# Kernel optimization log

Hardware: AMD Instinct MI355X
Metric: run time of the kernel (lower is better)

Reference implementation:

```python
import jax, jax.numpy as jnp
import numpy as np

K = 16          # neighbors per query (args.k)
EPS_NORM = 1e-5  # LayerNorm / BatchNorm eps (torch default)


def _knn_edges(xyz, B, n):
    # batch-aware kNN: equal-sized batches, edges never cross batch boundary
    x = xyz.reshape(B, n, 3)
    d2 = jnp.sum((x[:, :, None, :] - x[:, None, :, :]) ** 2, -1)   # [B,n,n]
    _, idx = jax.lax.top_k(-d2, K)                                 # [B,n,K] local neighbor ids
    col = (idx + (jnp.arange(B) * n)[:, None, None]).reshape(-1)   # source (neighbor) [E]
    row = jnp.repeat(jnp.arange(B * n), K)                         # target (query)    [E]
    return row, col


def _forward(support_xyz, batch_index, features, lang_features, mask_flattened,
             W1, b1, ln_g, ln_b, W2, b2,
             Wl1, bl1, bn_g, bn_b, Wl2, bl2,
             Wr1, br1, Wr2, br2, row, col):
    N = support_xyz.shape[0]
    B, L, Fl = lang_features.shape
    # feat_encoder: Linear -> LayerNorm -> ReLU -> Linear
    h = features @ W1 + b1
    mu = h.mean(-1, keepdims=True)
    var = ((h - mu) ** 2).mean(-1, keepdims=True)
    h = (h - mu) / jnp.sqrt(var + EPS_NORM) * ln_g + ln_b
    feats = jax.nn.relu(h) @ W2 + b2                               # [N,F]
    # lang_encoder: Linear -> BatchNorm1d (batch statistics) -> ReLU -> Linear
    hl = lang_features.reshape(B * L, Fl) @ Wl1 + bl1
    mul = hl.mean(0)
    varl = ((hl - mul) ** 2).mean(0)
    hl = (hl - mul) / jnp.sqrt(varl + EPS_NORM) * bn_g + bn_b
    lang = (jax.nn.relu(hl) @ Wl2 + bl2).reshape(B, L, -1)         # [B,L,F]
    lang_flat = lang[batch_index]                                  # [N,L,F]
    # per-point / per-token attention logits
    atten = jnp.einsum('nf,nlf->nl', feats, lang_flat)             # [N,L]
    # segment softmax over incoming kNN edges (CenterOp max / add)
    attenmax = jax.ops.segment_max(atten[col], row, num_segments=N, indices_are_sorted=True)
    a = jnp.exp(atten[col] - attenmax[row])                        # [E,L]
    attensum = jax.ops.segment_sum(a, row, num_segments=N, indices_are_sorted=True)
    # CenterConv message
    att = a / attensum[row] * mask_flattened[row]                  # [E,L]
    att = att / (att.sum(-1, keepdims=True) + 1e-7)
    ctx = jnp.einsum('el,elf->ef', att, lang_flat[col])            # [E,F] attended lang feat
    xi, xj = support_xyz[row], support_xyz[col]
    d = xi - xj
    nrm = jnp.sqrt(jnp.sum(d * d, -1, keepdims=True) + 1e-12)
    ew = jnp.concatenate([xi, xj, d, nrm], -1)                     # [E,10]
    ew = jax.nn.relu(ew @ Wr1 + br1) @ Wr2 + br2                   # [E,F] rel_encoder
    msg = feats[col] * ctx * ew                                    # [E,F]
    rel = jax.ops.segment_sum(msg, row, num_segments=N, indices_are_sorted=True)
    return feats + rel


def setup_inputs() -> dict:
    key = jax.random.key(0)
    ks = jax.random.split(key, 12)
    B, n, L = 4, 1024, 16
    N = B * n
    Fv, Fl, F = 256, 768, 128
    def w(k, shp, fan):
        return jax.random.normal(k, shp, jnp.float32) / np.sqrt(fan).astype(np.float32)
    mask = (jax.random.uniform(ks[3], (N, L)) < 0.8).astype(jnp.float32).at[:, 0].set(1.0)
    return {
        'support_xyz': jax.random.normal(ks[0], (N, 3), jnp.float32),
        'batch_index': jnp.repeat(jnp.arange(B), n),
        'features': jax.random.normal(ks[1], (N, Fv), jnp.float32),
        'lang_features': jax.random.normal(ks[2], (B, L, Fl), jnp.float32),
        'mask_flattened': mask,
        'W1': w(ks[4], (Fv, F), Fv), 'b1': jnp.zeros(F, jnp.float32),
        'ln_g': jnp.ones(F, jnp.float32), 'ln_b': jnp.zeros(F, jnp.float32),
        'W2': w(ks[5], (F, F), F), 'b2': jnp.zeros(F, jnp.float32),
        'Wl1': w(ks[6], (Fl, F), Fl), 'bl1': jnp.zeros(F, jnp.float32),
        'bn_g': jnp.ones(F, jnp.float32), 'bn_b': jnp.zeros(F, jnp.float32),
        'Wl2': w(ks[7], (F, F), F), 'bl2': jnp.zeros(F, jnp.float32),
        'Wr1': w(ks[8], (10, 64), 10), 'br1': jnp.zeros(64, jnp.float32),
        'Wr2': w(ks[9], (64, F), 64), 'br2': jnp.zeros(F, jnp.float32),
    }


def reference(support_xyz, batch_index, features, lang_features, mask_flattened,
              W1, b1, ln_g, ln_b, W2, b2,
              Wl1, bl1, bn_g, bn_b, Wl2, bl2,
              Wr1, br1, Wr2, br2):
    B = lang_features.shape[0]
    n = support_xyz.shape[0] // B
    row, col = _knn_edges(support_xyz, B, n)
    return _forward(support_xyz, batch_index, features, lang_features, mask_flattened,
                    W1, b1, ln_g, ln_b, W2, b2,
                    Wl1, bl1, bn_g, bn_b, Wl2, bl2,
                    Wr1, br1, Wr2, br2, row, col)
```

## Files before the change

kernel.cpp:

```cpp
#include <hip/hip_runtime.h>

typedef unsigned long long u64;
typedef short short8 __attribute__((ext_vector_type(8)));
typedef short short4v __attribute__((ext_vector_type(4)));
typedef float f32x4 __attribute__((ext_vector_type(4)));

#define N_PTS   4096
#define B_SZ    4
#define N_PER_B 1024
#define L_TOK   16
#define FV      256
#define FL      768
#define FDIM    128
#define KNN     16
#define RH      64

#define FINS 264
#define RBS  136
#define FBS  132

__device__ __forceinline__ short f2bf(float f) {
    unsigned int x = __float_as_uint(f);
    unsigned int r = (x + 0x7fffu + ((x >> 16) & 1u)) >> 16;
    return (short)r;
}
__device__ __forceinline__ float bf2f(short s) {
    return __uint_as_float(((unsigned int)(unsigned short)s) << 16);
}

__global__ __launch_bounds__(256) void kA_kernel(const float* __restrict__ xyz,
                                                 const float* __restrict__ lf,
                                                 const float* __restrict__ Wl1,
                                                 const float* __restrict__ bl1,
                                                 const float* __restrict__ Wr2,
                                                 const float* __restrict__ W1,
                                                 const float* __restrict__ W2,
                                                 int* __restrict__ knn,
                                                 float* __restrict__ hl,
                                                 short* __restrict__ wr2t,
                                                 short* __restrict__ w1t_hi,
                                                 short* __restrict__ w1t_lo,
                                                 short* __restrict__ w2t_hi,
                                                 short* __restrict__ w2t_lo) {
    __shared__ float smem[1024];
    int b = blockIdx.x, t = threadIdx.x;

    if (b < 1024) {
        int lane = t & 63;
        int q = b * 4 + (t >> 6);
        int base = (q >> 10) << 10;
        float qx = xyz[q * 3 + 0];
        float qy = xyz[q * 3 + 1];
        float qz = xyz[q * 3 + 2];
        u64 keys[16];
#pragma unroll
        for (int m = 0; m < 16; m++) {
            int j = base + lane + (m << 6);
            float dx = qx - xyz[j * 3 + 0];
            float dy = qy - xyz[j * 3 + 1];
            float dz = qz - xyz[j * 3 + 2];
            float d2 = __fadd_rn(__fadd_rn(__fmul_rn(dx, dx), __fmul_rn(dy, dy)),
                                 __fmul_rn(dz, dz));
            keys[m] = (((u64)__float_as_uint(d2)) << 32) | (unsigned int)j;
        }
        for (int r = 0; r < KNN; r++) {
            u64 lmin = keys[0];
#pragma unroll
            for (int m = 1; m < 16; m++) lmin = (keys[m] < lmin) ? keys[m] : lmin;
            u64 g = lmin;
#pragma unroll
            for (int off = 32; off > 0; off >>= 1) {
                u64 o = __shfl_xor(g, off, 64);
                g = (o < g) ? o : g;
            }
#pragma unroll
            for (int m = 0; m < 16; m++)
                if (keys[m] == g) keys[m] = ~0ULL;
            if (lane == 0) knn[q * KNN + r] = (int)(g & 0xffffffffu);
        }
    } else if (b < 1088) {
        int r = b - 1024;
        float* lrow = smem;
        float* part = smem + 768;
        for (int k = t; k < FL; k += 256) lrow[k] = lf[r * FL + k];
        __syncthreads();
        int c = t & 127, kh = t >> 7;
        float acc = (kh == 0) ? bl1[c] : 0.f;
        int k0 = kh * 384;
#pragma unroll 8
        for (int k = k0; k < k0 + 384; k++) acc += lrow[k] * Wl1[k * FDIM + c];
        part[kh * FDIM + c] = acc;
        __syncthreads();
        if (kh == 0) hl[r * FDIM + c] = part[c] + part[FDIM + c];
    } else if (b == 1088) {
        for (int p = t; p < RH * FDIM; p += 256) {
            int c = p >> 6, k = p & 63;
            wr2t[c * RH + k] = f2bf(Wr2[k * FDIM + c]);
        }
    } else if (b == 1089) {
        for (int p = t; p < FDIM * FDIM; p += 256) {
            int k = p >> 7, c = p & 127;
            float v = W2[p];
            short h = f2bf(v);
            w2t_hi[c * FDIM + k] = h;
            w2t_lo[c * FDIM + k] = f2bf(v - bf2f(h));
        }
    } else {
        int kbase = (b - 1090) * 128;
        for (int p = t; p < 128 * FDIM; p += 256) {
            int k = kbase + (p >> 7), c = p & 127;
            float v = W1[k * FDIM + c];
            short h = f2bf(v);
            w1t_hi[c * FV + k] = h;
            w1t_lo[c * FV + k] = f2bf(v - bf2f(h));
        }
    }
}

__global__ __launch_bounds__(128) void lang2_kernel(const float* __restrict__ hl,
                                                    const float* __restrict__ bn_g,
                                                    const float* __restrict__ bn_b,
                                                    const float* __restrict__ Wl2,
                                                    const float* __restrict__ bl2,
                                                    float* __restrict__ lang,
                                                    short* __restrict__ langT) {
    __shared__ float rl4[4][FDIM];
    int t = threadIdx.x;
    int r0 = blockIdx.x * 4;
    float s = 0.f, s2 = 0.f;
#pragma unroll 8
    for (int r = 0; r < 64; r++) {
        float v = hl[r * FDIM + t];
        s += v; s2 += v * v;
    }
    float mu = s * (1.f / 64.f);
    float var = s2 * (1.f / 64.f) - mu * mu;
    float rs = rsqrtf(var + 1e-5f);
    float g = bn_g[t], bb = bn_b[t];
#pragma unroll
    for (int p = 0; p < 4; p++)
        rl4[p][t] = fmaxf((hl[(r0 + p) * FDIM + t] - mu) * rs * g + bb, 0.f);
    __syncthreads();
    float bv = bl2[t];
    float a[4] = {bv, bv, bv, bv};
#pragma unroll 8
    for (int k = 0; k < FDIM; k++) {
        float w = Wl2[k * FDIM + t];
        a[0] += rl4[0][k] * w;
        a[1] += rl4[1][k] * w;
        a[2] += rl4[2][k] * w;
        a[3] += rl4[3][k] * w;
    }
#pragma unroll
    for (int p = 0; p < 4; p++) {
        int r = r0 + p;
        lang[r * FDIM + t] = a[p];
        langT[((r >> 4) * FDIM + t) * L_TOK + (r & 15)] = f2bf(a[p]);
    }
}

__global__ __launch_bounds__(256) void feat_kernel(const float* __restrict__ features,
                                                   const float* __restrict__ b1,
                                                   const float* __restrict__ ln_g,
                                                   const float* __restrict__ ln_b,
                                                   const float* __restrict__ b2,
                                                   const short* __restrict__ w1t_hi,
                                                   const short* __restrict__ w1t_lo,
                                                   const short* __restrict__ w2t_hi,
                                                   const short* __restrict__ w2t_lo,
                                                   const float* __restrict__ lang,
                                                   float* __restrict__ feats,
                                                   float* __restrict__ atten) {
    __shared__ short fin_hi[16 * FINS], fin_lo[16 * FINS];
    __shared__ short rb_hi[16 * RBS], rb_lo[16 * RBS];
    __shared__ float fbuf[16 * FBS];
    __shared__ float red_s[4 * 16], red_q[4 * 16];
    int t = threadIdx.x;
    int w = t >> 6, lane = t & 63, quad = lane >> 4, e16 = lane & 15;
    int i0 = blockIdx.x * 16;

    {
        const float4* src = (const float4*)(features + i0 * FV);
#pragma unroll
        for (int v = 0; v < 4; v++) {
            int flat = t + 256 * v;
            float4 x = src[flat];
            int p = flat >> 6, k = (flat & 63) * 4;
            short4v hi, lo;
            hi[0] = f2bf(x.x); lo[0] = f2bf(x.x - bf2f(hi[0]));
            hi[1] = f2bf(x.y); lo[1] = f2bf(x.y - bf2f(hi[1]));
            hi[2] = f2bf(x.z); lo[2] = f2bf(x.z - bf2f(hi[2]));
            hi[3] = f2bf(x.w); lo[3] = f2bf(x.w - bf2f(hi[3]));
            *(short4v*)&fin_hi[p * FINS + k] = hi;
            *(short4v*)&fin_lo[p * FINS + k] = lo;
        }
    }
    __syncthreads();

    int c0 = 32 * w + e16, c1 = c0 + 16;

    f32x4 acc0 = {0.f, 0.f, 0.f, 0.f}, acc1 = {0.f, 0.f, 0.f, 0.f};
#pragma unroll
    for (int s = 0; s < 8; s++) {
        int ko = s * 32 + quad * 8;
        short8 Ah = *(const short8*)&fin_hi[e16 * FINS + ko];
        short8 Al = *(const short8*)&fin_lo[e16 * FINS + ko];
        short8 B0h = *(const short8*)&w1t_hi[c0 * FV + ko];
        short8 B0l = *(const short8*)&w1t_lo[c0 * FV + ko];
        short8 B1h = *(const short8*)&w1t_hi[c1 * FV + ko];
        short8 B1l = *(const short8*)&w1t_lo[c1 * FV + ko];
        acc0 = __builtin_amdgcn_mfma_f32_16x16x32_bf16(Ah, B0h, acc0, 0, 0, 0);
        acc0 = __builtin_amdgcn_mfma_f32_16x16x32_bf16(Ah, B0l, acc0, 0, 0, 0);
        acc0 = __builtin_amdgcn_mfma_f32_16x16x32_bf16(Al, B0h, acc0, 0, 0, 0);
        acc1 = __builtin_amdgcn_mfma_f32_16x16x32_bf16(Ah, B1h, acc1, 0, 0, 0);
        acc1 = __builtin_amdgcn_mfma_f32_16x16x32_bf16(Ah, B1l, acc1, 0, 0, 0);
        acc1 = __builtin_amdgcn_mfma_f32_16x16x32_bf16(Al, B1h, acc1, 0, 0, 0);
    }
    float b1c0 = b1[c0], b1c1 = b1[c1];
    float h0[4], h1[4], sp[4], qp[4];
#pragma unroll
    for (int r = 0; r < 4; r++) {
        h0[r] = acc0[r] + b1c0;
        h1[r] = acc1[r] + b1c1;
        sp[r] = h0[r] + h1[r];
        qp[r] = h0[r] * h0[r] + h1[r] * h1[r];
    }
#pragma unroll
    for (int off = 1; off < 16; off <<= 1) {
#pragma unroll
        for (int r = 0; r < 4; r++) {
            sp[r] += __shfl_xor(sp[r], off, 16);
            qp[r] += __shfl_xor(qp[r], off, 16);
        }
    }
    if (e16 == 0) {
#pragma unroll
        for (int r = 0; r < 4; r++) {
            red_s[w * 16 + quad * 4 + r] = sp[r];
            red_q[w * 16 + quad * 4 + r] = qp[r];
        }
    }
    __syncthreads();
    float g0 = ln_g[c0], g1 = ln_g[c1], be0 = ln_b[c0], be1 = ln_b[c1];
#pragma unroll
    for (int r = 0; r < 4; r++) {
        int p = quad * 4 + r;
        float S = red_s[p] + red_s[16 + p] + red_s[32 + p] + red_s[48 + p];
        float Q = red_q[p] + red_q[16 + p] + red_q[32 + p] + red_q[48 + p];
        float mu = S * (1.f / 128.f);
        float var = Q * (1.f / 128.f) - mu * mu;
        float rs = rsqrtf(var + 1e-5f);
        float r0 = fmaxf((h0[r] - mu) * rs * g0 + be0, 0.f);
        float r1 = fmaxf((h1[r] - mu) * rs * g1 + be1, 0.f);
        short hh;
        hh = f2bf(r0); rb_hi[p * RBS + c0] = hh; rb_lo[p * RBS + c0] = f2bf(r0 - bf2f(hh));
        hh = f2bf(r1); rb_hi[p * RBS + c1] = hh; rb_lo[p * RBS + c1] = f2bf(r1 - bf2f(hh));
    }
    __syncthreads();

    f32x4 o0 = {0.f, 0.f, 0.f, 0.f}, o1 = {0.f, 0.f, 0.f, 0.f};
#pragma unroll
    for (int s = 0; s < 4; s++) {
        int ko = s * 32 + quad * 8;
        short8 Ah = *(const short8*)&rb_hi[e16 * RBS + ko];
        short8 Al = *(const short8*)&rb_lo[e16 * RBS + ko];
        short8 B0h = *(const short8*)&w2t_hi[c0 * FDIM + ko];
        short8 B0l = *(const short8*)&w2t_lo[c0 * FDIM + ko];
        short8 B1h = *(const short8*)&w2t_hi[c1 * FDIM + ko];
        short8 B1l = *(const short8*)&w2t_lo[c1 * FDIM + ko];
        o0 = __builtin_amdgcn_mfma_f32_16x16x32_bf16(Ah, B0h, o0, 0, 0, 0);
        o0 = __builtin_amdgcn_mfma_f32_16x16x32_bf16(Ah, B0l, o0, 0, 0, 0);
        o0 = __builtin_amdgcn_mfma_f32_16x16x32_bf16(Al, B0h, o0, 0, 0, 0);
        o1 = __builtin_amdgcn_mfma_f32_16x16x32_bf16(Ah, B1h, o1, 0, 0, 0);
        o1 = __builtin_amdgcn_mfma_f32_16x16x32_bf16(Ah, B1l, o1, 0, 0, 0);
        o1 = __builtin_amdgcn_mfma_f32_16x16x32_bf16(Al, B1h, o1, 0, 0, 0);
    }
    float b20 = b2[c0], b21 = b2[c1];
#pragma unroll
    for (int r = 0; r < 4; r++) {
        int p = quad * 4 + r;
        float f0 = o0[r] + b20, f1 = o1[r] + b21;
        feats[(i0 + p) * FDIM + c0] = f0;
        feats[(i0 + p) * FDIM + c1] = f1;
        fbuf[p * FBS + c0] = f0;
        fbuf[p * FBS + c1] = f1;
    }
    __syncthreads();

    int pp = t >> 4, l = t & 15;
    int bi = i0 >> 10;
    const float4* lr = (const float4*)(lang + (bi * L_TOK + l) * FDIM);
    float acc = 0.f;
#pragma unroll
    for (int k = 0; k < FDIM / 4; k++) {
        float4 x = lr[k];
        float4 y = *(const float4*)&fbuf[pp * FBS + 4 * k];
        acc += x.x * y.x + x.y * y.y + x.z * y.z + x.w * y.w;
    }
    atten[(i0 + pp) * L_TOK + l] = acc;
}

__global__ __launch_bounds__(256) void edge_kernel(const float* __restrict__ xyz,
                                                   const float* __restrict__ mask,
                                                   const float* __restrict__ Wr1,
                                                   const float* __restrict__ br1,
                                                   const short* __restrict__ wr2t,
                                                   const float* __restrict__ br2,
                                                   const int* __restrict__ knn,
                                                   const short* __restrict__ langT,
                                                   const float* __restrict__ feats,
                                                   const float* __restrict__ atten,
                                                   float* __restrict__ out) {
    int lane = threadIdx.x & 63;
    int wid  = threadIdx.x >> 6;
    int i    = blockIdx.x * 4 + wid;
    int bi   = i >> 10;
    int quad = lane >> 4;
    int e16  = lane & 15;

    int idxe = knn[i * KNN + e16];

    float sat[8];
    if (quad < 2) {
        const float4* ap = (const float4*)(atten + idxe * L_TOK + quad * 8);
        float4 a0 = ap[0], a1 = ap[1];
        sat[0] = a0.x; sat[1] = a0.y; sat[2] = a0.z; sat[3] = a0.w;
        sat[4] = a1.x; sat[5] = a1.y; sat[6] = a1.z; sat[7] = a1.w;
    } else {
#pragma unroll
        for (int j = 0; j < 8; j++) sat[j] = 0.f;
    }

    float mx[8];
#pragma unroll
    for (int j = 0; j < 8; j++) mx[j] = sat[j];
#pragma unroll
    for (int off = 1; off < 16; off <<= 1) {
#pragma unroll
        for (int j = 0; j < 8; j++) mx[j] = fmaxf(mx[j], __shfl_xor(mx[j], off, 16));
    }
    float ex[8], sm[8];
#pragma unroll
    for (int j = 0; j < 8; j++) { ex[j] = __expf(sat[j] - mx[j]); sm[j] = ex[j]; }
#pragma unroll
    for (int off = 1; off < 16; off <<= 1) {
#pragma unroll
        for (int j = 0; j < 8; j++) sm[j] += __shfl_xor(sm[j], off, 16);
    }
    float st[8];
    if (quad < 2) {
        const float4* mp = (const float4*)(mask + i * L_TOK + quad * 8);
        float4 m0 = mp[0], m1 = mp[1];
        float mv[8] = {m0.x, m0.y, m0.z, m0.w, m1.x, m1.y, m1.z, m1.w};
#pragma unroll
        for (int j = 0; j < 8; j++) st[j] = ex[j] * (mv[j] / sm[j]);
    } else {
#pragma unroll
        for (int j = 0; j < 8; j++) st[j] = 0.f;
    }
    float s = st[0] + st[1] + st[2] + st[3] + st[4] + st[5] + st[6] + st[7];
    s += __shfl_xor(s, 16, 64);
    s += __shfl_xor(s, 32, 64);
    float inv2 = 1.f / (s + 1e-7f);
    short8 sattA;
#pragma unroll
    for (int j = 0; j < 8; j++) sattA[j] = f2bf(st[j] * inv2);

    float xi0 = xyz[i * 3 + 0], xi1 = xyz[i * 3 + 1], xi2 = xyz[i * 3 + 2];
    float xj0 = xyz[idxe * 3 + 0], xj1 = xyz[idxe * 3 + 1], xj2 = xyz[idxe * 3 + 2];
    float d0 = xi0 - xj0, d1 = xi1 - xj1, d2v = xi2 - xj2;
    float nr = sqrtf(d0 * d0 + d1 * d1 + d2v * d2v + 1e-12f);
    float ein[10] = {xi0, xi1, xi2, xj0, xj1, xj2, d0, d1, d2v, nr};
    short8 hidA[2];
#pragma unroll
    for (int sstep = 0; sstep < 2; sstep++) {
        int k0 = sstep * 32 + quad * 8;
        float h[8];
        const float4* bp = (const float4*)(br1 + k0);
        float4 b0 = bp[0], b1v = bp[1];
        h[0] = b0.x; h[1] = b0.y; h[2] = b0.z; h[3] = b0.w;
        h[4] = b1v.x; h[5] = b1v.y; h[6] = b1v.z; h[7] = b1v.w;
#pragma unroll
        for (int m = 0; m < 10; m++) {
            const float4* wp = (const float4*)(Wr1 + m * RH + k0);
            float4 w0 = wp[0], w1 = wp[1];
            float em = ein[m];
            h[0] += em * w0.x; h[1] += em * w0.y; h[2] += em * w0.z; h[3] += em * w0.w;
            h[4] += em * w1.x; h[5] += em * w1.y; h[6] += em * w1.z; h[7] += em * w1.w;
        }
#pragma unroll
        for (int j = 0; j < 8; j++) hidA[sstep][j] = f2bf(fmaxf(h[j], 0.f));
    }

    int idxr[4];
#pragma unroll
    for (int r = 0; r < 4; r++) idxr[r] = knn[i * KNN + quad * 4 + r];

#pragma unroll 2
    for (int tile = 0; tile < 8; tile++) {
        int cc = tile * 16 + e16;
        const short8* w2p = (const short8*)(wr2t + cc * RH);
        f32x4 accew = {0.f, 0.f, 0.f, 0.f};
        accew = __builtin_amdgcn_mfma_f32_16x16x32_bf16(hidA[0], w2p[quad],     accew, 0, 0, 0);
        accew = __builtin_amdgcn_mfma_f32_16x16x32_bf16(hidA[1], w2p[4 + quad], accew, 0, 0, 0);
        short8 lsB;
        if (quad < 2) {
            lsB = ((const short8*)(langT + (bi * FDIM + cc) * L_TOK))[quad];
        } else {
#pragma unroll
            for (int j = 0; j < 8; j++) lsB[j] = 0;
        }
        f32x4 accctx = {0.f, 0.f, 0.f, 0.f};
        accctx = __builtin_amdgcn_mfma_f32_16x16x32_bf16(sattA, lsB, accctx, 0, 0, 0);

        float br2c = br2[cc];
        float msum = 0.f;
#pragma unroll
        for (int r = 0; r < 4; r++) {
            float fj = feats[idxr[r] * FDIM + cc];
            msum += fj * accctx[r] * (accew[r] + br2c);
        }
        msum += __shfl_xor(msum, 16, 64);
        msum += __shfl_xor(msum, 32, 64);
        if (lane < 16)
            out[i * FDIM + cc] = feats[i * FDIM + cc] + msum;
    }
}

extern "C" void kernel_launch(void* const* d_in, const int* in_sizes, int n_in,
                              void* d_out, int out_size, void* d_ws, size_t ws_size,
                              hipStream_t stream) {
    const float* xyz   = (const float*)d_in[0];
    const float* features = (const float*)d_in[2];
    const float* lang_f   = (const float*)d_in[3];
    const float* mask     = (const float*)d_in[4];
    const float* W1   = (const float*)d_in[5];
    const float* b1   = (const float*)d_in[6];
    const float* ln_g = (const float*)d_in[7];
    const float* ln_b = (const float*)d_in[8];
    const float* W2   = (const float*)d_in[9];
    const float* b2   = (const float*)d_in[10];
    const float* Wl1  = (const float*)d_in[11];
    const float* bl1  = (const float*)d_in[12];
    const float* bn_g = (const float*)d_in[13];
    const float* bn_b = (const float*)d_in[14];
    const float* Wl2  = (const float*)d_in[15];
    const float* bl2  = (const float*)d_in[16];
    const float* Wr1  = (const float*)d_in[17];
    const float* br1  = (const float*)d_in[18];
    const float* Wr2  = (const float*)d_in[19];
    const float* br2  = (const float*)d_in[20];

    float* ws_feats = (float*)d_ws;
    float* ws_atten = ws_feats + N_PTS * FDIM;
    float* ws_lang  = ws_atten + N_PTS * L_TOK;
    float* ws_hl    = ws_lang + B_SZ * L_TOK * FDIM;
    int*   ws_knn   = (int*)(ws_hl + 64 * FDIM);
    short* ws_wr2t  = (short*)(ws_knn + N_PTS * KNN);
    short* ws_langT = ws_wr2t + FDIM * RH;
    short* ws_w1t_hi = ws_langT + B_SZ * FDIM * L_TOK;
    short* ws_w1t_lo = ws_w1t_hi + FDIM * FV;
    short* ws_w2t_hi = ws_w1t_lo + FDIM * FV;
    short* ws_w2t_lo = ws_w2t_hi + FDIM * FDIM;

    kA_kernel<<<1092, 256, 0, stream>>>(xyz, lang_f, Wl1, bl1, Wr2, W1, W2,
                                        ws_knn, ws_hl, ws_wr2t,
                                        ws_w1t_hi, ws_w1t_lo, ws_w2t_hi, ws_w2t_lo);
    lang2_kernel<<<16, 128, 0, stream>>>(ws_hl, bn_g, bn_b, Wl2, bl2,
                                         ws_lang, ws_langT);
    feat_kernel<<<N_PTS / 16, 256, 0, stream>>>(features, b1, ln_g, ln_b, b2,
                                                ws_w1t_hi, ws_w1t_lo,
                                                ws_w2t_hi, ws_w2t_lo,
                                                ws_lang, ws_feats, ws_atten);
    edge_kernel<<<N_PTS / 4, 256, 0, stream>>>(xyz, mask, Wr1, br1, ws_wr2t, br2,
                                               ws_knn, ws_langT, ws_feats, ws_atten,
                                               (float*)d_out);
}
```

Baseline: 174.1 us.

## Replace iterative kNN argmin rounds with wave-wide radix select using ballots

The per-query 16-round min-extraction is replaced. The old version did 64-bit key compares and cross-lane shuffle reductions in each round. The new version runs a bitwise radix select over the 32-bit distance keys, counting candidates with ballot and popcount to find the 16th-smallest threshold. It then compacts the selected neighbor indices with mbcnt prefix counts. This cuts per-lane 64-bit work and shuffle traffic, but neighbors are now emitted in index order rather than distance order, which only matters if downstream code depends on edge ordering.

```diff
diff --git a/kernel.cpp b/kernel.cpp
--- a/kernel.cpp
+++ b/kernel.cpp
@@ -26,6 +26,10 @@
 }
 __device__ __forceinline__ float bf2f(short s) {
     return __uint_as_float(((unsigned int)(unsigned short)s) << 16);
+}
+__device__ __forceinline__ int mbcnt64(u64 m) {
+    return __builtin_amdgcn_mbcnt_hi((unsigned)(m >> 32),
+                                     __builtin_amdgcn_mbcnt_lo((unsigned)m, 0));
 }
 
 __global__ __launch_bounds__(256) void kA_kernel(const float* __restrict__ xyz,
@@ -52,7 +56,7 @@
         float qx = xyz[q * 3 + 0];
         float qy = xyz[q * 3 + 1];
         float qz = xyz[q * 3 + 2];
-        u64 keys[16];
+        unsigned keys[16], xk[16];
 #pragma unroll
         for (int m = 0; m < 16; m++) {
             int j = base + lane + (m << 6);
@@ -61,22 +65,49 @@
             float dz = qz - xyz[j * 3 + 2];
             float d2 = __fadd_rn(__fadd_rn(__fmul_rn(dx, dx), __fmul_rn(dy, dy)),
                                  __fmul_rn(dz, dz));
-            keys[m] = (((u64)__float_as_uint(d2)) << 32) | (unsigned int)j;
-        }
-        for (int r = 0; r < KNN; r++) {
-            u64 lmin = keys[0];
-#pragma unroll
-            for (int m = 1; m < 16; m++) lmin = (keys[m] < lmin) ? keys[m] : lmin;
-            u64 g = lmin;
-#pragma unroll
-            for (int off = 32; off > 0; off >>= 1) {
-                u64 o = __shfl_xor(g, off, 64);
-                g = (o < g) ? o : g;
+            keys[m] = __float_as_uint(d2);
+            xk[m] = keys[m];
+        }
+        unsigned prefix = 0;
+        int need = 16;
+#pragma unroll
+        for (int bit = 30; bit >= 0; --bit) {
+            unsigned lim = 1u << bit;
+            int c = 0;
+#pragma unroll
+            for (int m = 0; m < 16; m++)
+                c += __popcll(__ballot(xk[m] < lim));
+            if (c < need) {
+                need -= c;
+                prefix |= lim;
+#pragma unroll
+                for (int m = 0; m < 16; m++) xk[m] ^= lim;
             }
-#pragma unroll
-            for (int m = 0; m < 16; m++)
-                if (keys[m] == g) keys[m] = ~0ULL;
-            if (lane == 0) knn[q * KNN + r] = (int)(g & 0xffffffffu);
+        }
+        int pos = 0;
+#pragma unroll
+        for (int m = 0; m < 16; m++) {
+            bool less = keys[m] < prefix;
+            bool eqv  = (xk[m] == 0);
+            u64 em = __ballot(eqv);
+            bool take_eq = false;
+            if (need > 0) {
+                int ec = __popcll(em);
+                if (ec <= need) {
+                    take_eq = eqv;
+                    need -= ec;
+                } else {
+                    take_eq = eqv && (mbcnt64(em) < need);
+                    need = 0;
+                }
+            }
+            bool sel = less || take_eq;
+            u64 sm = __ballot(sel);
+            if (sel) {
+                int my = pos + mbcnt64(sm);
+                knn[q * KNN + my] = base + lane + (m << 6);
+            }
+            pos += __popcll(sm);
         }
     } else if (b < 1088) {
         int r = b - 1024;
```

New measurement: 171.2 us. Within noise of the previous version (-1.7%).
